# Kernel tuning notes

Hardware: AMD Instinct MI355X
Metric: run time of the kernel (lower is better)

The kernel has to match this reference:

```python
import jax, jax.numpy as jnp
import numpy as np

B, H, W, C = 64, 56, 56, 256
ROUTES = 4
CONV_OUT = 64
BN_EPS = 1e-3  # keras BatchNormalization default epsilon


def setup_inputs() -> dict:
    key = jax.random.key(0)
    ks = jax.random.split(key, 8)
    inputs = jax.random.normal(ks[0], (B, H, W, C), jnp.float32)
    gamma = jnp.ones((C,), jnp.float32)
    beta = jnp.zeros((C,), jnp.float32)
    moving_mean = 0.1 * jax.random.normal(ks[1], (C,), jnp.float32)
    moving_var = jax.random.uniform(ks[2], (C,), jnp.float32, 0.5, 1.5)
    conv_w = 0.02 * jax.random.normal(ks[3], (3, 3, C, CONV_OUT), jnp.float32)  # HWIO
    conv_b = jnp.zeros((CONV_OUT,), jnp.float32)
    fc_w = 0.05 * jax.random.normal(ks[4], (CONV_OUT, ROUTES), jnp.float32)
    fc_b = jnp.zeros((ROUTES,), jnp.float32)
    return {"inputs": inputs, "gamma": gamma, "beta": beta,
            "moving_mean": moving_mean, "moving_var": moving_var,
            "conv_w": conv_w, "conv_b": conv_b, "fc_w": fc_w, "fc_b": fc_b}


def reference(inputs, gamma, beta, moving_mean, moving_var, conv_w, conv_b, fc_w, fc_b):
    # BatchNormalization in inference mode (training=None -> moving stats)
    rx = (inputs - moving_mean) * jax.lax.rsqrt(moving_var + BN_EPS) * gamma + beta
    # Conv2D(64, 3x3, stride 2, padding 'same'), NHWC / HWIO
    rx = jax.lax.conv_general_dilated(
        rx, conv_w, window_strides=(2, 2), padding="SAME",
        dimension_numbers=("NHWC", "HWIO", "NHWC")) + conv_b
    # GlobalAveragePooling2D -> [B, 64]
    rx = jnp.mean(rx, axis=(1, 2))
    # Dense(routes) -> routing logits [B, ROUTES]
    routing_x = rx @ fc_w + fc_b
    # choose_route: top-1 route, direct per-sample channel slice (no dense mask)
    route_width = C // ROUTES
    route = jnp.argmax(routing_x, axis=-1)  # [B]
    ch_idx = route[:, None] * route_width + jnp.arange(route_width)  # [B, rw]
    idx = ch_idx[:, None, None, :]  # [B,1,1,rw] broadcasts over H, W
    x = jnp.take_along_axis(inputs, idx, axis=3)  # [B, H, W, rw]
    return x, routing_x
```

## Files before the change

### kernel.cpp

```cpp
#include <hip/hip_runtime.h>

#define B 64
#define H 56
#define W 56
#define C 256
#define ROUTES 4
#define CONV_OUT 64
#define BN_EPS 0.001f
#define RW (C / ROUTES)
#define X_SIZE ((long)B * H * W * RW)

#define P2_FLOATS ((long)B * H * 3 * C)
#define OFFU P2_FLOATS
#define U_FLOATS (10L * C * 4)
#define OFFROUTE (OFFU + U_FLOATS)

typedef float floatx4 __attribute__((ext_vector_type(4)));

__device__ __forceinline__ void f4add(float4& a, const float4& v) {
    a.x += v.x; a.y += v.y; a.z += v.z; a.w += v.w;
}

__global__ __launch_bounds__(256) void k_reduce(const float* __restrict__ x,
                                                const float* __restrict__ gamma,
                                                const float* __restrict__ beta,
                                                const float* __restrict__ mmean,
                                                const float* __restrict__ mvar,
                                                const float* __restrict__ conv_w,
                                                const float* __restrict__ fc_w,
                                                float* __restrict__ ws) {
    int tid = threadIdx.x;

    if (blockIdx.x >= B * H) {
        __shared__ float fcw_s[CONV_OUT * ROUTES];
        fcw_s[tid] = fc_w[tid];
        __syncthreads();

        int c = (blockIdx.x - B * H) * 64 + (tid >> 2);
        int r = tid & 3;

        float t[9];
        #pragma unroll
        for (int k = 0; k < 9; ++k) {
            const float4* w4 = (const float4*)conv_w + ((long)(k * C + c) * CONV_OUT) / 4;
            float s = 0.f;
            #pragma unroll
            for (int o4 = 0; o4 < 16; ++o4) {
                float4 wv = w4[o4];
                s += wv.x * fcw_s[(o4 * 4 + 0) * 4 + r];
                s += wv.y * fcw_s[(o4 * 4 + 1) * 4 + r];
                s += wv.z * fcw_s[(o4 * 4 + 2) * 4 + r];
                s += wv.w * fcw_s[(o4 * 4 + 3) * 4 + r];
            }
            t[k] = s;
        }

        float a  = gamma[c] * rsqrtf(mvar[c] + BN_EPS);
        float bb = beta[c] - mmean[c] * a;

        float u[10];
        u[0] =  t[0] + t[2] + t[6] + t[8];
        u[1] =  t[1] + t[7];
        u[2] =  t[3] + t[5];
        u[3] =  t[4];
        u[4] = -(t[2] + t[8]);
        u[5] = -t[5];
        u[6] = -(t[6] + t[8]);
        u[7] = -t[7];
        u[8] =  t[8];
        u[9] = 784.f * (t[0] + t[1] + t[3] + t[4])
             + 756.f * (t[2] + t[5] + t[6] + t[7])
             + 729.f * t[8];

        float* U = ws + OFFU;
        float sa = a * (1.f / 784.f);
        #pragma unroll
        for (int j = 0; j < 9; ++j) U[(j * C + c) * 4 + r] = sa * u[j];
        U[(9 * C + c) * 4 + r] = bb * (1.f / 784.f) * u[9];
        return;
    }

    int blk = blockIdx.x;
    int cg = tid & 63;
    int wg = tid >> 6;

    const float4* xv = (const float4*)x;
    long base = (long)blk * W * (C / 4) + cg;

    float4 v[14];
    #pragma unroll
    for (int i = 0; i < 14; ++i) v[i] = xv[base + (long)(wg + 4 * i) * (C / 4)];

    float4 a4 = {0,0,0,0}, b4 = {0,0,0,0};
    #pragma unroll
    for (int i = 0; i < 14; i += 2) { f4add(a4, v[i]); f4add(b4, v[i + 1]); }
    f4add(a4, b4);

    __shared__ float4 lds[4][64];
    lds[wg][cg] = a4;
    __syncthreads();

    float4* P2 = (float4*)ws + (long)blk * 3 * 64;
    if (wg == 0) {
        float4 e = lds[0][cg]; f4add(e, lds[2][cg]);
        P2[cg]       = e;
        P2[128 + cg] = v[0];
    } else if (wg == 1) {
        float4 o = lds[1][cg]; f4add(o, lds[3][cg]);
        P2[64 + cg]  = o;
    }
}

__global__ __launch_bounds__(256) void k_route(const float* __restrict__ ws,
                                               const float* __restrict__ conv_b,
                                               const float* __restrict__ fc_w,
                                               const float* __restrict__ fc_b,
                                               float* __restrict__ out_routing,
                                               int* __restrict__ route) {
    __shared__ floatx4 red[256];
    __shared__ float rxs[ROUTES];

    int b = blockIdx.x;
    int c = threadIdx.x;
    const float* Pb = ws + (long)b * H * 3 * C;

    float See = 0.f, Seo = 0.f, c0e = 0.f;
    float Soe = 0.f, Soo = 0.f, c0o = 0.f;
    #pragma unroll 4
    for (int h = 0; h < H; h += 2) {
        const float* re = Pb + (long)h * 3 * C + c;
        See += re[0];
        Seo += re[C];
        c0e += re[2 * C];
        Soe += re[3 * C];
        Soo += re[4 * C];
        c0o += re[5 * C];
    }
    float r0e = Pb[c];
    float r0o = Pb[C + c];
    float x00 = Pb[2 * C + c];

    float Pj[9] = {See, Seo, Soe, Soo, c0e, c0o, r0e, r0o, x00};

    const floatx4* U4 = (const floatx4*)(ws + OFFU);
    floatx4 v = U4[9 * C + c];
    #pragma unroll
    for (int j = 0; j < 9; ++j) v += Pj[j] * U4[j * C + c];

    red[c] = v;
    __syncthreads();
    #pragma unroll
    for (int s = 128; s >= 1; s >>= 1) {
        if (c < s) red[c] += red[c + s];
        __syncthreads();
    }

    if (c < ROUTES) {
        float cst = fc_b[c];
        for (int o = 0; o < CONV_OUT; ++o) cst += conv_b[o] * fc_w[o * ROUTES + c];
        float val = red[0][c] + cst;
        rxs[c] = val;
        out_routing[b * ROUTES + c] = val;
    }
    __syncthreads();
    if (c == 0) {
        int best = 0;
        for (int r = 1; r < ROUTES; ++r) if (rxs[r] > rxs[best]) best = r;
        route[b] = best;
    }
}

__global__ __launch_bounds__(256) void k_gather(const float* __restrict__ x,
                                                const int* __restrict__ route,
                                                float* __restrict__ out) {
    long base4 = (long)blockIdx.x * 1024 + threadIdx.x;
    int b = blockIdx.x / 49;
    int rt = route[b];
    const floatx4* xv = (const floatx4*)x;
    #pragma unroll
    for (int m = 0; m < 4; ++m) {
        long idx = base4 + m * 256;
        int j = (int)(idx & 15);
        long pixel = idx >> 4;
        floatx4 v = xv[pixel * (C / 4) + (long)rt * (RW / 4) + j];
        __builtin_nontemporal_store(v, &((floatx4*)out)[idx]);
    }
}

extern "C" void kernel_launch(void* const* d_in, const int* in_sizes, int n_in,
                              void* d_out, int out_size, void* d_ws, size_t ws_size,
                              hipStream_t stream) {
    const float* inputs = (const float*)d_in[0];
    const float* gamma  = (const float*)d_in[1];
    const float* beta   = (const float*)d_in[2];
    const float* mmean  = (const float*)d_in[3];
    const float* mvar   = (const float*)d_in[4];
    const float* conv_w = (const float*)d_in[5];
    const float* conv_b = (const float*)d_in[6];
    const float* fc_w   = (const float*)d_in[7];
    const float* fc_b   = (const float*)d_in[8];

    float* out   = (float*)d_out;
    float* ws    = (float*)d_ws;
    int*   route = (int*)((char*)d_ws + OFFROUTE * sizeof(float));

    k_reduce<<<B * H + 4, 256, 0, stream>>>(inputs, gamma, beta, mmean, mvar,
                                            conv_w, fc_w, ws);
    k_route<<<B, 256, 0, stream>>>(ws, conv_b, fc_w, fc_b, out + X_SIZE, route);
    k_gather<<<3136, 256, 0, stream>>>(inputs, route, out);
}
```

Measured before the change: 328.0 us.

## Fuse routing into reduce kernel via per-batch last-block atomic counter

Removes the separate k_route launch and the precomputed U table blocks. Each reduce block increments a per-batch atomic counter, and the last of the 56 blocks for a batch recomputes the folded conv/fc weights and does the routing reduction in place. This saves one kernel launch and the dependency bubble between the two kernels. In exchange, 64 winner blocks each redo the 9x64 weight folding per channel, and correctness depends on the counter never being reset, relying on a modulo 56 check.

New measurement: 817.5 us. +149.2%, slower.

```diff
diff --git a/kernel.cpp b/kernel.cpp
--- a/kernel.cpp
+++ b/kernel.cpp
@@ -11,9 +11,8 @@
 #define X_SIZE ((long)B * H * W * RW)
 
 #define P2_FLOATS ((long)B * H * 3 * C)
-#define OFFU P2_FLOATS
-#define U_FLOATS (10L * C * 4)
-#define OFFROUTE (OFFU + U_FLOATS)
+#define OFFROUTE P2_FLOATS
+#define OFFCNT (P2_FLOATS + B)
 
 typedef float floatx4 __attribute__((ext_vector_type(4)));
 
@@ -27,60 +26,22 @@
                                                 const float* __restrict__ mmean,
                                                 const float* __restrict__ mvar,
                                                 const float* __restrict__ conv_w,
+                                                const float* __restrict__ conv_b,
                                                 const float* __restrict__ fc_w,
-                                                float* __restrict__ ws) {
+                                                const float* __restrict__ fc_b,
+                                                float* __restrict__ ws,
+                                                float* __restrict__ out_routing,
+                                                int* __restrict__ route,
+                                                unsigned* __restrict__ cnt) {
+    __shared__ float4 lds[4][64];
+    __shared__ float fcw_s[CONV_OUT * ROUTES];
+    __shared__ floatx4 red[256];
+    __shared__ float rxs[ROUTES];
+    __shared__ int winflag;
+
     int tid = threadIdx.x;
-
-    if (blockIdx.x >= B * H) {
-        __shared__ float fcw_s[CONV_OUT * ROUTES];
-        fcw_s[tid] = fc_w[tid];
-        __syncthreads();
-
-        int c = (blockIdx.x - B * H) * 64 + (tid >> 2);
-        int r = tid & 3;
-
-        float t[9];
-        #pragma unroll
-        for (int k = 0; k < 9; ++k) {
-            const float4* w4 = (const float4*)conv_w + ((long)(k * C + c) * CONV_OUT) / 4;
-            float s = 0.f;
-            #pragma unroll
-            for (int o4 = 0; o4 < 16; ++o4) {
-                float4 wv = w4[o4];
-                s += wv.x * fcw_s[(o4 * 4 + 0) * 4 + r];
-                s += wv.y * fcw_s[(o4 * 4 + 1) * 4 + r];
-                s += wv.z * fcw_s[(o4 * 4 + 2) * 4 + r];
-                s += wv.w * fcw_s[(o4 * 4 + 3) * 4 + r];
-            }
-            t[k] = s;
-        }
-
-        float a  = gamma[c] * rsqrtf(mvar[c] + BN_EPS);
-        float bb = beta[c] - mmean[c] * a;
-
-        float u[10];
-        u[0] =  t[0] + t[2] + t[6] + t[8];
-        u[1] =  t[1] + t[7];
-        u[2] =  t[3] + t[5];
-        u[3] =  t[4];
-        u[4] = -(t[2] + t[8]);
-        u[5] = -t[5];
-        u[6] = -(t[6] + t[8]);
-        u[7] = -t[7];
-        u[8] =  t[8];
-        u[9] = 784.f * (t[0] + t[1] + t[3] + t[4])
-             + 756.f * (t[2] + t[5] + t[6] + t[7])
-             + 729.f * t[8];
-
-        float* U = ws + OFFU;
-        float sa = a * (1.f / 784.f);
-        #pragma unroll
-        for (int j = 0; j < 9; ++j) U[(j * C + c) * 4 + r] = sa * u[j];
-        U[(9 * C + c) * 4 + r] = bb * (1.f / 784.f) * u[9];
-        return;
-    }
-
     int blk = blockIdx.x;
+    int b = blk / H;
     int cg = tid & 63;
     int wg = tid >> 6;
 
@@ -96,7 +57,6 @@
     for (int i = 0; i < 14; i += 2) { f4add(a4, v[i]); f4add(b4, v[i + 1]); }
     f4add(a4, b4);
 
-    __shared__ float4 lds[4][64];
     lds[wg][cg] = a4;
     __syncthreads();
 
@@ -109,21 +69,57 @@
         float4 o = lds[1][cg]; f4add(o, lds[3][cg]);
         P2[64 + cg]  = o;
     }
-}
-
-__global__ __launch_bounds__(256) void k_route(const float* __restrict__ ws,
-                                               const float* __restrict__ conv_b,
-                                               const float* __restrict__ fc_w,
-                                               const float* __restrict__ fc_b,
-                                               float* __restrict__ out_routing,
-                                               int* __restrict__ route) {
-    __shared__ floatx4 red[256];
-    __shared__ float rxs[ROUTES];
-
-    int b = blockIdx.x;
-    int c = threadIdx.x;
+
+    __syncthreads();
+    if (tid == 0) {
+        unsigned old = __hip_atomic_fetch_add(&cnt[b], 1u, __ATOMIC_ACQ_REL,
+                                              __HIP_MEMORY_SCOPE_AGENT);
+        winflag = ((old % 56u) == 55u);
+    }
+    __syncthreads();
+    if (!winflag) return;
+
+    __threadfence();
+    fcw_s[tid] = fc_w[tid];
+    __syncthreads();
+
+    int c = tid;
+    const floatx4* f4 = (const floatx4*)fcw_s;
+
+    floatx4 t[9];
+    #pragma unroll
+    for (int k = 0; k < 9; ++k) {
+        const float4* w4 = (const float4*)conv_w + ((long)(k * C + c) * CONV_OUT) / 4;
+        floatx4 s = {0,0,0,0};
+        #pragma unroll
+        for (int o4 = 0; o4 < 16; ++o4) {
+            float4 wv = w4[o4];
+            s += wv.x * f4[o4 * 4 + 0];
+            s += wv.y * f4[o4 * 4 + 1];
+            s += wv.z * f4[o4 * 4 + 2];
+            s += wv.w * f4[o4 * 4 + 3];
+        }
+        t[k] = s;
+    }
+
+    float a  = gamma[c] * rsqrtf(mvar[c] + BN_EPS);
+    float bb = beta[c] - mmean[c] * a;
+
+    floatx4 u[10];
+    u[0] =  t[0] + t[2] + t[6] + t[8];
+    u[1] =  t[1] + t[7];
+    u[2] =  t[3] + t[5];
+    u[3] =  t[4];
+    u[4] = -(t[2] + t[8]);
+    u[5] = -t[5];
+    u[6] = -(t[6] + t[8]);
+    u[7] = -t[7];
+    u[8] =  t[8];
+    u[9] = 784.f * (t[0] + t[1] + t[3] + t[4])
+         + 756.f * (t[2] + t[5] + t[6] + t[7])
+         + 729.f * t[8];
+
     const float* Pb = ws + (long)b * H * 3 * C;
-
     float See = 0.f, Seo = 0.f, c0e = 0.f;
     float Soe = 0.f, Soo = 0.f, c0o = 0.f;
     #pragma unroll 4
@@ -142,12 +138,12 @@
 
     float Pj[9] = {See, Seo, Soe, Soo, c0e, c0o, r0e, r0o, x00};
 
-    const floatx4* U4 = (const floatx4*)(ws + OFFU);
-    floatx4 v = U4[9 * C + c];
-    #pragma unroll
-    for (int j = 0; j < 9; ++j) v += Pj[j] * U4[j * C + c];
-
-    red[c] = v;
+    float sa = a * (1.f / 784.f);
+    floatx4 vv = (bb * (1.f / 784.f)) * u[9];
+    #pragma unroll
+    for (int j = 0; j < 9; ++j) vv += Pj[j] * (sa * u[j]);
+
+    red[c] = vv;
     __syncthreads();
     #pragma unroll
     for (int s = 128; s >= 1; s >>= 1) {
@@ -200,12 +196,13 @@
     const float* fc_w   = (const float*)d_in[7];
     const float* fc_b   = (const float*)d_in[8];
 
-    float* out   = (float*)d_out;
-    float* ws    = (float*)d_ws;
-    int*   route = (int*)((char*)d_ws + OFFROUTE * sizeof(float));
-
-    k_reduce<<<B * H + 4, 256, 0, stream>>>(inputs, gamma, beta, mmean, mvar,
-                                            conv_w, fc_w, ws);
-    k_route<<<B, 256, 0, stream>>>(ws, conv_b, fc_w, fc_b, out + X_SIZE, route);
+    float* out      = (float*)d_out;
+    float* ws       = (float*)d_ws;
+    int*   route    = (int*)((char*)d_ws + OFFROUTE * sizeof(float));
+    unsigned* cnt   = (unsigned*)((char*)d_ws + OFFCNT * sizeof(float));
+
+    k_reduce<<<B * H, 256, 0, stream>>>(inputs, gamma, beta, mmean, mvar,
+                                        conv_w, conv_b, fc_w, fc_b,
+                                        ws, out + X_SIZE, route, cnt);
     k_gather<<<3136, 256, 0, stream>>>(inputs, route, out);
 }
```
